# Performance work log

Measured on AMD Instinct MI355X. Metric: run time of the kernel, lower is better.

## Reference

```python
import jax, jax.numpy as jnp
import numpy as np
import math

D_MODEL = 64
N_HEAD = 8
BATCH = 16
NTOK = 511  # pads to 512 in original torch code; padn = 1 > 0


def setup_inputs() -> dict:
    key = jax.random.key(0)
    ks = jax.random.split(key, 4)
    scl = 0.005
    x = jax.random.normal(ks[0], (BATCH, NTOK, D_MODEL), jnp.float32)
    wq_w = scl * jax.random.normal(ks[1], (N_HEAD * D_MODEL, D_MODEL + 1), jnp.float32)
    wq_w = wq_w.at[:, -1].set(0.0)  # bias column zeroed at init
    wv_w = scl * jax.random.normal(ks[2], (N_HEAD * D_MODEL, D_MODEL + 1), jnp.float32)
    wv_w = wv_w.at[:, -1].set(0.0)
    wk = scl * jnp.ones((N_HEAD, D_MODEL), jnp.float32)
    fanout_w = scl * jax.random.normal(ks[3], (D_MODEL, D_MODEL + 1), jnp.float32)
    fanout_w = fanout_w.at[:, -1].set(0.0)
    return {"x": x, "wq_w": wq_w, "wv_w": wv_w, "wk": wk, "fanout_w": fanout_w}


def _linear_m(w, x):
    # LinearM: w[:, :-1] is weight, w[:, -1] is bias
    return jnp.einsum('oi,bti->bto', w[:, :-1], x) + w[:, -1]


def _l1_logits(q, k):
    # q, k: [b, t, h, w]. Returns [b, s(key), d(query), h] =
    #   -(1/sqrt(w)) * sum_w |q[b,d,h,w] - k[b,s,h,w]|
    # Scan over the width axis so we never materialize a [b,t,t,h,w] tensor.
    b, t, h, w = q.shape
    scale = 1.0 / math.sqrt(w)
    qw = jnp.moveaxis(q, -1, 0)  # [w, b, t, h]
    kw = jnp.moveaxis(k, -1, 0)

    def body(acc, qk):
        qi, ki = qk  # each [b, t, h]
        return acc + jnp.abs(qi[:, None, :, :] - ki[:, :, None, :]), None

    acc0 = jnp.zeros((b, t, t, h), q.dtype)
    acc, _ = jax.lax.scan(body, acc0, (qw, kw))
    return -acc * scale


def reference(x, wq_w, wv_w, wk, fanout_w):
    b, t, dm = x.shape
    q = _linear_m(wq_w, x).reshape(b, t, N_HEAD, D_MODEL)
    v = _linear_m(wv_w, x).reshape(b, t, N_HEAD, D_MODEL)
    # k: x broadcast over heads, elementwise-gated by wk
    k = x[:, :, None, :] * wk[None, None, :, :]  # [b, t, h, w]
    logits = _l1_logits(q, k)  # [b, s, d, h]
    # Extra zero-logit 'sink' key row (the original zero-padded row with a[:,t,:,:]=0)
    sink = jnp.zeros((b, 1, t, N_HEAD), logits.dtype)
    logits = jnp.concatenate([logits, sink], axis=1)  # [b, t+1, d, h]
    a = jax.nn.softmax(logits, axis=1)[:, :t]  # softmax over keys+sink, drop sink
    # einsum 'bsdh,bshw->bdhw' then sum over h, fused:
    out = jnp.einsum('bsdh,bshw->bdw', a, v)  # [b, t, d_model]
    y = jax.nn.relu(out)  # module's self.gelu is actually nn.ReLU()
    y = _linear_m(fanout_w, y)
    return x + y
```

## Files before the change

kernel.cpp:

```cpp
#include <hip/hip_runtime.h>
#include <stdint.h>


#define B  16
#define H  8
#define T  511

typedef __fp16 f16x2 __attribute__((ext_vector_type(2)));
typedef __fp16 f16x8 __attribute__((ext_vector_type(8)));
typedef float  f32x4 __attribute__((ext_vector_type(4)));

#if __has_builtin(__builtin_amdgcn_exp2f)
#define EXP2F(x) __builtin_amdgcn_exp2f(x)
#else
#define EXP2F(x) exp2f(x)
#endif

__device__ __forceinline__ uint32_t SAD(uint32_t a, uint32_t b, uint32_t c) {
#if __has_builtin(__builtin_amdgcn_sad_u8)
  return __builtin_amdgcn_sad_u8(a, b, c);
#else
  uint32_t d;
  asm("v_sad_u8 %0, %1, %2, %3" : "=v"(d) : "v"(a), "v"(b), "v"(c));
  return d;
#endif
}

__device__ __forceinline__ uint32_t PKRTZ(float a, float b) {
  f16x2 r = __builtin_amdgcn_cvt_pkrtz(a, b);
  return __builtin_bit_cast(uint32_t, r);
}

__device__ __forceinline__ uint32_t quantu8(float v) {
  float q = __builtin_rintf(__builtin_fmaf(v, 256.f, 128.f));
  q = fminf(fmaxf(q, 0.f), 255.f);
  return (uint32_t)(int)q;
}

__global__ void wtrans_kernel(const float* __restrict__ wq, const float* __restrict__ wv,
                              const float* __restrict__ wf, float* __restrict__ wt,
                              float* __restrict__ bias, float* __restrict__ wft,
                              float* __restrict__ biasf) {
  const int idx = blockIdx.x * 256 + (int)threadIdx.x;
  if (idx < 64 * 1024) {
    const int k = idx >> 10, j = idx & 1023;
    const float* src = (j < 512) ? wq : wv;
    const int oc = j & 511;
    wt[idx] = src[oc * 65 + k];
    if (k == 0) bias[j] = src[oc * 65 + 64];
  } else if (idx < 64 * 1024 + 64 * 64) {
    const int r = idx - 64 * 1024;
    const int k = r >> 6, w = r & 63;
    wft[r] = wf[w * 65 + k];
    if (k == 0) biasf[w] = wf[w * 65 + 64];
  }
}

__global__ void __launch_bounds__(256, 2) proj_kernel(
    const float* __restrict__ x, const float* __restrict__ wt,
    const float* __restrict__ bias, const float* __restrict__ wk,
    uint8_t* __restrict__ qq, _Float16* __restrict__ vt,
    uint8_t* __restrict__ kq) {
  __shared__ float xt[64][16];
  const int b = blockIdx.y, tc = blockIdx.x;
  const int t0 = tc * 16;
  const int tid = threadIdx.x;
  {
    const int tl = tid >> 4, k0 = (tid & 15) * 4;
    const int t = t0 + tl;
    float4 v = {0.f, 0.f, 0.f, 0.f};
    if (t < T) v = *(const float4*)(x + ((size_t)b * T + t) * 64 + k0);
    xt[k0 + 0][tl] = v.x; xt[k0 + 1][tl] = v.y;
    xt[k0 + 2][tl] = v.z; xt[k0 + 3][tl] = v.w;
  }
  __syncthreads();
  const int j0 = tid * 4;
  const float4 bs = *(const float4*)(bias + j0);
  float4 acc[16];
#pragma unroll
  for (int t = 0; t < 16; ++t) acc[t] = bs;
  for (int k = 0; k < 64; ++k) {
    const float4 w4 = *(const float4*)(wt + (size_t)k * 1024 + j0);
    const float4* xr = (const float4*)xt[k];
    const float4 xa = xr[0], xb = xr[1], xc = xr[2], xd = xr[3];
    const float xv[16] = {xa.x, xa.y, xa.z, xa.w, xb.x, xb.y, xb.z, xb.w,
                          xc.x, xc.y, xc.z, xc.w, xd.x, xd.y, xd.z, xd.w};
#pragma unroll
    for (int t = 0; t < 16; ++t) {
      acc[t].x = __builtin_fmaf(w4.x, xv[t], acc[t].x);
      acc[t].y = __builtin_fmaf(w4.y, xv[t], acc[t].y);
      acc[t].z = __builtin_fmaf(w4.z, xv[t], acc[t].z);
      acc[t].w = __builtin_fmaf(w4.w, xv[t], acc[t].w);
    }
  }
  const int oc = j0 & 511;
  const int hh = oc >> 6, w0 = oc & 63;
  const size_t bh = (size_t)b * H + hh;
  if (j0 < 512) {
#pragma unroll
    for (int t = 0; t < 16; ++t) {
      if (t0 + t < T) {
        const uint32_t u = quantu8(acc[t].x) | (quantu8(acc[t].y) << 8) |
                           (quantu8(acc[t].z) << 16) | (quantu8(acc[t].w) << 24);
        *(uint32_t*)(qq + (bh * T + (size_t)(t0 + t)) * 64 + w0) = u;
      }
    }
  } else {
#pragma unroll
    for (int i = 0; i < 4; ++i) {
      uint32_t u[8];
      const float* a = (const float*)acc;
#pragma unroll
      for (int m = 0; m < 8; ++m) u[m] = PKRTZ(a[4 * (2 * m) + i], a[4 * (2 * m + 1) + i]);
      _Float16* p = vt + (bh * 64 + (size_t)(w0 + i)) * 512 + t0;
      *(uint4*)(p)     = make_uint4(u[0], u[1], u[2], u[3]);
      *(uint4*)(p + 8) = make_uint4(u[4], u[5], u[6], u[7]);
    }
  }
  const int tk = tid >> 4, w4 = (tid & 15) * 4;
  if (t0 + tk < T) {
    const float xv0 = xt[w4 + 0][tk], xv1 = xt[w4 + 1][tk];
    const float xv2 = xt[w4 + 2][tk], xv3 = xt[w4 + 3][tk];
#pragma unroll
    for (int hh2 = 0; hh2 < H; ++hh2) {
      const float4 wkv = *(const float4*)(wk + hh2 * 64 + w4);
      const uint32_t u = quantu8(xv0 * wkv.x) | (quantu8(xv1 * wkv.y) << 8) |
                         (quantu8(xv2 * wkv.z) << 16) | (quantu8(xv3 * wkv.w) << 24);
      *(uint32_t*)(kq + (((size_t)b * H + hh2) * T + (size_t)(t0 + tk)) * 64 + w4) = u;
    }
  }
}

__global__ void __launch_bounds__(512, 2) attn_kernel(
    const uint8_t* __restrict__ qq, const uint8_t* __restrict__ kq,
    const _Float16* __restrict__ vt, _Float16* __restrict__ anum) {
  __shared__ uint4 klds[2048];
  __shared__ float dend[4][4][16];
  const int qt = blockIdx.x, h = blockIdx.y, b = blockIdx.z;
  const int bh = b * H + h;
  const int tid = threadIdx.x;
  {
    const uint4* kg = (const uint4*)(kq + (size_t)bh * T * 64);
    for (int i = tid; i < T * 4; i += 512) {
      const int s = i >> 2, j = i & 3;
      klds[s * 4 + (j ^ ((s >> 3) & 3))] = kg[i];
    }
  }
  const int wave = tid >> 6, lane = tid & 63;
  const int pair = wave & 3, khalf = wave >> 2;
  const int c = lane & 15, g = lane >> 4;
  const int qb = qt * 256 + pair * 64;
  uint4 q[4][4];
#pragma unroll
  for (int m = 0; m < 4; ++m) {
    const int qm = qb + 16 * m + c;
    const int qsafe = qm < T ? qm : T - 1;
    const uint4* qp = (const uint4*)(qq + ((size_t)bh * T + qsafe) * 64);
#pragma unroll
    for (int i = 0; i < 4; ++i) q[m][i] = qp[i];
  }
  const _Float16* vb = vt + (size_t)bh * 64 * 512;
  f32x4 acc[4][4];
#pragma unroll
  for (int m = 0; m < 4; ++m)
#pragma unroll
    for (int nt = 0; nt < 4; ++nt) acc[m][nt] = f32x4{0.f, 0.f, 0.f, 0.f};
  float den[4] = {0.f, 0.f, 0.f, 0.f};
  const float Cl = -0x1.715476p+0f / 2048.0f;
  __syncthreads();

#pragma unroll 1
  for (int kt = 0; kt < 8; ++kt) {
    const int ks = khalf * 256 + kt * 32;
    const _Float16* vp0 = vb + (size_t)c * 512 + ks + g * 8;
    uint4 bvec[4];
#pragma unroll
    for (int nt = 0; nt < 4; ++nt) bvec[nt] = *(const uint4*)(vp0 + nt * 16 * 512);
    uint32_t pk[4][4];
#pragma unroll
    for (int jj = 0; jj < 4; ++jj) {
      float pp[4][2];
#pragma unroll
      for (int e = 0; e < 2; ++e) {
        const int s = ks + g * 8 + jj * 2 + e;
        const int sr = s < T ? s : T - 1;
        const uint4* kp = klds + sr * 4;
        const int bb = (sr >> 3) & 3;
        const uint4 k0 = kp[bb], k1 = kp[1 ^ bb], k2 = kp[2 ^ bb], k3 = kp[3 ^ bb];
        const bool live = s < T;
#pragma unroll
        for (int m = 0; m < 4; ++m) {
          uint32_t a0 = 0, a1 = 0;
          a0 = SAD(q[m][0].x, k0.x, a0); a0 = SAD(q[m][0].y, k0.y, a0);
          a0 = SAD(q[m][0].z, k0.z, a0); a0 = SAD(q[m][0].w, k0.w, a0);
          a0 = SAD(q[m][1].x, k1.x, a0); a0 = SAD(q[m][1].y, k1.y, a0);
          a0 = SAD(q[m][1].z, k1.z, a0); a0 = SAD(q[m][1].w, k1.w, a0);
          a1 = SAD(q[m][2].x, k2.x, a1); a1 = SAD(q[m][2].y, k2.y, a1);
          a1 = SAD(q[m][2].z, k2.z, a1); a1 = SAD(q[m][2].w, k2.w, a1);
          a1 = SAD(q[m][3].x, k3.x, a1); a1 = SAD(q[m][3].y, k3.y, a1);
          a1 = SAD(q[m][3].z, k3.z, a1); a1 = SAD(q[m][3].w, k3.w, a1);
          const float p = EXP2F((float)(a0 + a1) * Cl);
          pp[m][e] = live ? p : 0.f;
        }
      }
#pragma unroll
      for (int m = 0; m < 4; ++m) {
        den[m] += pp[m][0] + pp[m][1];
        pk[m][jj] = PKRTZ(pp[m][0], pp[m][1]);
      }
    }
#pragma unroll
    for (int m = 0; m < 4; ++m) {
      const f16x8 af = __builtin_bit_cast(f16x8, make_uint4(pk[m][0], pk[m][1], pk[m][2], pk[m][3]));
#pragma unroll
      for (int nt = 0; nt < 4; ++nt) {
        const f16x8 bf = __builtin_bit_cast(f16x8, bvec[nt]);
        acc[m][nt] = __builtin_amdgcn_mfma_f32_16x16x32_f16(af, bf, acc[m][nt], 0, 0, 0);
      }
    }
  }

#pragma unroll
  for (int m = 0; m < 4; ++m) {
    den[m] += __shfl_xor(den[m], 16, 64);
    den[m] += __shfl_xor(den[m], 32, 64);
  }

  __syncthreads();
  uint32_t* scr = (uint32_t*)klds;
  if (khalf) {
#pragma unroll
    for (int m = 0; m < 4; ++m) {
      if (g == 0) dend[pair][m][c] = den[m];
#pragma unroll
      for (int nt = 0; nt < 4; ++nt) {
        const int j = m * 8 + nt * 2;
        scr[j * 256 + pair * 64 + lane]       = PKRTZ(acc[m][nt][0], acc[m][nt][1]);
        scr[(j + 1) * 256 + pair * 64 + lane] = PKRTZ(acc[m][nt][2], acc[m][nt][3]);
      }
    }
  }
  __syncthreads();
  if (!khalf) {
    float dtot[4];
#pragma unroll
    for (int m = 0; m < 4; ++m) dtot[m] = den[m] + dend[pair][m][c] + 1.0f;
#pragma unroll
    for (int m = 0; m < 4; ++m) {
#pragma unroll
      for (int nt = 0; nt < 4; ++nt) {
        const int j = m * 8 + nt * 2;
        const f16x2 u0 = __builtin_bit_cast(f16x2, scr[j * 256 + pair * 64 + lane]);
        const f16x2 u1 = __builtin_bit_cast(f16x2, scr[(j + 1) * 256 + pair * 64 + lane]);
        acc[m][nt][0] += (float)u0[0]; acc[m][nt][1] += (float)u0[1];
        acc[m][nt][2] += (float)u1[0]; acc[m][nt][3] += (float)u1[1];
      }
    }
#pragma unroll
    for (int m = 0; m < 4; ++m) {
#pragma unroll
      for (int r = 0; r < 4; ++r) {
        const float rd = 1.0f / __shfl(dtot[m], g * 4 + r, 64);
        const int qr = qb + 16 * m + g * 4 + r;
        if (qr < T) {
          _Float16* ap = anum + (((size_t)b * T + qr) * H + h) * 64 + c;
          ap[0]  = (_Float16)(acc[m][0][r] * rd);
          ap[16] = (_Float16)(acc[m][1][r] * rd);
          ap[32] = (_Float16)(acc[m][2][r] * rd);
          ap[48] = (_Float16)(acc[m][3][r] * rd);
        }
      }
    }
  }
}

__global__ void __launch_bounds__(256) finalize_kernel(
    const float* __restrict__ x, const _Float16* __restrict__ anum,
    const float* __restrict__ wft, const float* __restrict__ biasf,
    float* __restrict__ out) {
  __shared__ float u[4][64];
  const int tid = threadIdx.x;
  const int lt = tid >> 6, w = tid & 63;
  const int gt = blockIdx.x * 4 + lt;
  const _Float16* an = anum + (size_t)gt * H * 64 + w;
  float s = 0.f;
#pragma unroll
  for (int hh = 0; hh < H; ++hh) s += (float)an[hh * 64];
  u[lt][w] = fmaxf(s, 0.f);
  __syncthreads();
  float y = biasf[w];
#pragma unroll 8
  for (int k = 0; k < 64; ++k) y = __builtin_fmaf(wft[k * 64 + w], u[lt][k], y);
  out[(size_t)gt * 64 + w] = x[(size_t)gt * 64 + w] + y;
}

extern "C" void kernel_launch(void* const* d_in, const int* in_sizes, int n_in,
                              void* d_out, int out_size, void* d_ws, size_t ws_size,
                              hipStream_t stream) {
  (void)in_sizes; (void)n_in; (void)out_size; (void)ws_size;
  const float* x  = (const float*)d_in[0];
  const float* wq = (const float*)d_in[1];
  const float* wv = (const float*)d_in[2];
  const float* wk = (const float*)d_in[3];
  const float* wf = (const float*)d_in[4];
  float* out = (float*)d_out;

  uint8_t* ws = (uint8_t*)d_ws;
  const size_t o_qq   = 0;
  const size_t o_kq   = 4186112;
  const size_t o_vt   = 8372224;
  const size_t o_anum = 16760832;
  const size_t o_wt   = 25133056;
  const size_t o_bias = 25395200;
  const size_t o_wft  = 25399296;
  const size_t o_bf   = 25415680;

  uint8_t*  qq    = ws + o_qq;
  uint8_t*  kq    = ws + o_kq;
  _Float16* vt    = (_Float16*)(ws + o_vt);
  _Float16* anum  = (_Float16*)(ws + o_anum);
  float*    wt    = (float*)(ws + o_wt);
  float*    bias  = (float*)(ws + o_bias);
  float*    wft   = (float*)(ws + o_wft);
  float*    biasf = (float*)(ws + o_bf);

  wtrans_kernel<<<dim3((64 * 1024 + 64 * 64 + 255) / 256), 256, 0, stream>>>(
      wq, wv, wf, wt, bias, wft, biasf);
  proj_kernel<<<dim3(32, B), 256, 0, stream>>>(x, wt, bias, wk, qq, vt, kq);
  attn_kernel<<<dim3(2, H, B), 512, 0, stream>>>(qq, kq, vt, anum);
  finalize_kernel<<<dim3(B * T / 4), 256, 0, stream>>>(x, anum, wft, biasf, out);
}
```

Baseline: 77.97 us.

## Split attention key range across three wave groups instead of two

The attention kernel now launches 768 threads per block and splits the 512 keys into three chunks of 160, 160 and 192, one per group of four waves, instead of two halves of 256. Partial numerators and denominators from groups 1 and 2 are written to LDS (klds reused plus a new 32KB scratch buffer) and reduced by group 0. The aim is more waves per block, and so more latency hiding and parallelism per CU, for the same 256 blocks. In exchange, LDS use per block rises, launch bounds are tighter (which can cause register spilling), and group 2 carries more work than the others, so the split is unbalanced.

Measured after the change: 87.36 us. +12.0%, slower.

```diff
diff --git a/kernel.cpp b/kernel.cpp
--- a/kernel.cpp
+++ b/kernel.cpp
@@ -131,23 +131,24 @@
   }
 }
 
-__global__ void __launch_bounds__(512, 2) attn_kernel(
+__global__ void __launch_bounds__(768, 3) attn_kernel(
     const uint8_t* __restrict__ qq, const uint8_t* __restrict__ kq,
     const _Float16* __restrict__ vt, _Float16* __restrict__ anum) {
   __shared__ uint4 klds[2048];
-  __shared__ float dend[4][4][16];
+  __shared__ uint32_t scr2[8192];
+  __shared__ float dend[2][4][4][16];
   const int qt = blockIdx.x, h = blockIdx.y, b = blockIdx.z;
   const int bh = b * H + h;
   const int tid = threadIdx.x;
   {
     const uint4* kg = (const uint4*)(kq + (size_t)bh * T * 64);
-    for (int i = tid; i < T * 4; i += 512) {
+    for (int i = tid; i < T * 4; i += 768) {
       const int s = i >> 2, j = i & 3;
       klds[s * 4 + (j ^ ((s >> 3) & 3))] = kg[i];
     }
   }
   const int wave = tid >> 6, lane = tid & 63;
-  const int pair = wave & 3, khalf = wave >> 2;
+  const int pair = wave & 3, ks = wave >> 2;
   const int c = lane & 15, g = lane >> 4;
   const int qb = qt * 256 + pair * 64;
   uint4 q[4][4];
@@ -167,12 +168,13 @@
     for (int nt = 0; nt < 4; ++nt) acc[m][nt] = f32x4{0.f, 0.f, 0.f, 0.f};
   float den[4] = {0.f, 0.f, 0.f, 0.f};
   const float Cl = -0x1.715476p+0f / 2048.0f;
+  const int kbeg = ks * 160;
+  const int kend = (ks == 2) ? 512 : kbeg + 160;
   __syncthreads();
 
 #pragma unroll 1
-  for (int kt = 0; kt < 8; ++kt) {
-    const int ks = khalf * 256 + kt * 32;
-    const _Float16* vp0 = vb + (size_t)c * 512 + ks + g * 8;
+  for (int s0 = kbeg; s0 < kend; s0 += 32) {
+    const _Float16* vp0 = vb + (size_t)c * 512 + s0 + g * 8;
     uint4 bvec[4];
 #pragma unroll
     for (int nt = 0; nt < 4; ++nt) bvec[nt] = *(const uint4*)(vp0 + nt * 16 * 512);
@@ -182,7 +184,7 @@
       float pp[4][2];
 #pragma unroll
       for (int e = 0; e < 2; ++e) {
-        const int s = ks + g * 8 + jj * 2 + e;
+        const int s = s0 + g * 8 + jj * 2 + e;
         const int sr = s < T ? s : T - 1;
         const uint4* kp = klds + sr * 4;
         const int bb = (sr >> 3) & 3;
@@ -227,33 +229,41 @@
   }
 
   __syncthreads();
-  uint32_t* scr = (uint32_t*)klds;
-  if (khalf) {
+  {
+    uint32_t* scr = (ks == 1) ? (uint32_t*)klds : scr2;
+    if (ks) {
+#pragma unroll
+      for (int m = 0; m < 4; ++m) {
+        if (g == 0) dend[ks - 1][pair][m][c] = den[m];
+#pragma unroll
+        for (int nt = 0; nt < 4; ++nt) {
+          const int j = m * 8 + nt * 2;
+          scr[j * 256 + pair * 64 + lane]       = PKRTZ(acc[m][nt][0], acc[m][nt][1]);
+          scr[(j + 1) * 256 + pair * 64 + lane] = PKRTZ(acc[m][nt][2], acc[m][nt][3]);
+        }
+      }
+    }
+  }
+  __syncthreads();
+  if (ks == 0) {
+    const uint32_t* s1 = (const uint32_t*)klds;
+    float dtot[4];
+#pragma unroll
+    for (int m = 0; m < 4; ++m)
+      dtot[m] = den[m] + dend[0][pair][m][c] + dend[1][pair][m][c] + 1.0f;
 #pragma unroll
     for (int m = 0; m < 4; ++m) {
-      if (g == 0) dend[pair][m][c] = den[m];
 #pragma unroll
       for (int nt = 0; nt < 4; ++nt) {
         const int j = m * 8 + nt * 2;
-        scr[j * 256 + pair * 64 + lane]       = PKRTZ(acc[m][nt][0], acc[m][nt][1]);
-        scr[(j + 1) * 256 + pair * 64 + lane] = PKRTZ(acc[m][nt][2], acc[m][nt][3]);
-      }
-    }
-  }
-  __syncthreads();
-  if (!khalf) {
-    float dtot[4];
-#pragma unroll
-    for (int m = 0; m < 4; ++m) dtot[m] = den[m] + dend[pair][m][c] + 1.0f;
-#pragma unroll
-    for (int m = 0; m < 4; ++m) {
-#pragma unroll
-      for (int nt = 0; nt < 4; ++nt) {
-        const int j = m * 8 + nt * 2;
-        const f16x2 u0 = __builtin_bit_cast(f16x2, scr[j * 256 + pair * 64 + lane]);
-        const f16x2 u1 = __builtin_bit_cast(f16x2, scr[(j + 1) * 256 + pair * 64 + lane]);
-        acc[m][nt][0] += (float)u0[0]; acc[m][nt][1] += (float)u0[1];
-        acc[m][nt][2] += (float)u1[0]; acc[m][nt][3] += (float)u1[1];
+        const f16x2 a0 = __builtin_bit_cast(f16x2, s1[j * 256 + pair * 64 + lane]);
+        const f16x2 a1 = __builtin_bit_cast(f16x2, s1[(j + 1) * 256 + pair * 64 + lane]);
+        const f16x2 b0 = __builtin_bit_cast(f16x2, scr2[j * 256 + pair * 64 + lane]);
+        const f16x2 b1 = __builtin_bit_cast(f16x2, scr2[(j + 1) * 256 + pair * 64 + lane]);
+        acc[m][nt][0] += (float)a0[0] + (float)b0[0];
+        acc[m][nt][1] += (float)a0[1] + (float)b0[1];
+        acc[m][nt][2] += (float)a1[0] + (float)b1[0];
+        acc[m][nt][3] += (float)a1[1] + (float)b1[1];
       }
     }
 #pragma unroll
@@ -327,6 +337,6 @@
   wtrans_kernel<<<dim3((64 * 1024 + 64 * 64 + 255) / 256), 256, 0, stream>>>(
       wq, wv, wf, wt, bias, wft, biasf);
   proj_kernel<<<dim3(32, B), 256, 0, stream>>>(x, wt, bias, wk, qq, vt, kq);
-  attn_kernel<<<dim3(2, H, B), 512, 0, stream>>>(qq, kq, vt, anum);
+  attn_kernel<<<dim3(2, H, B), 768, 0, stream>>>(qq, kq, vt, anum);
   finalize_kernel<<<dim3(B * T / 4), 256, 0, stream>>>(x, anum, wft, biasf, out);
 }
```
